# Performance work log

Hardware: AMD Instinct MI355X
Metric: run time of the kernel (lower is better)

## Reference

```python
import jax, jax.numpy as jnp
import numpy as np

DIM = 768
H = 16
HD = DIM // H  # 48


def setup_inputs() -> dict:
    key = jax.random.key(0)
    ks = jax.random.split(key, 9)
    s = 0.02
    return {
        "x": jax.random.normal(ks[0], (8, 1024, DIM), dtype=jnp.float32),
        "w_qkv": jax.random.normal(ks[1], (3 * DIM, DIM), dtype=jnp.float32) * s,
        "b_qkv": jax.random.normal(ks[2], (3 * DIM,), dtype=jnp.float32) * s,
        "w_l": jax.random.normal(ks[3], (H, H), dtype=jnp.float32) * 0.25,
        "b_l": jax.random.normal(ks[4], (H,), dtype=jnp.float32) * s,
        "w_w": jax.random.normal(ks[5], (H, H), dtype=jnp.float32) * 0.25,
        "b_w": jax.random.normal(ks[6], (H,), dtype=jnp.float32) * s,
        "w_proj": jax.random.normal(ks[7], (DIM, DIM), dtype=jnp.float32) * s,
        "b_proj": jax.random.normal(ks[8], (DIM,), dtype=jnp.float32) * s,
    }


def reference(x, w_qkv, b_qkv, w_l, b_l, w_w, b_w, w_proj, b_proj):
    B, N, C = x.shape
    scale = HD ** -0.5
    qkv = x @ w_qkv.T + b_qkv                        # [B,N,3C]
    qkv = qkv.reshape(B, N, 3, H, HD).transpose(2, 0, 3, 1, 4)  # [3,B,H,N,HD]
    q = qkv[0] * scale
    k = qkv[1]
    v = qkv[2]
    attn = jnp.einsum('bhqd,bhkd->bhqk', q, k)       # [B,H,N,N]
    # talking-heads mix before softmax (Linear over head dim)
    attn = jnp.einsum('bhqk,gh->bgqk', attn, w_l) + b_l[None, :, None, None]
    attn = jax.nn.softmax(attn, axis=-1)
    # talking-heads mix after softmax
    attn = jnp.einsum('bhqk,gh->bgqk', attn, w_w) + b_w[None, :, None, None]
    out = jnp.einsum('bhqk,bhkd->bhqd', attn, v)     # [B,H,N,HD]
    out = out.transpose(0, 2, 1, 3).reshape(B, N, C)
    return out @ w_proj.T + b_proj
```

## Files before the change

kernel.cpp:

```cpp
#include <hip/hip_runtime.h>

typedef unsigned short u16;
typedef unsigned int u32;
using short8 = __attribute__((__ext_vector_type__(8))) short;
using f32x4  = __attribute__((__ext_vector_type__(4))) float;

#define DIM 768
#define QKV3 2304
#define SEQ 1024
#define SCALE 0.14433756729740643f

__device__ __forceinline__ u16 f2bf(float f) {
  __bf16 h = (__bf16)f;
  u16 r;
  __builtin_memcpy(&r, &h, 2);
  return r;
}
__device__ __forceinline__ u32 packbf(float lo, float hi) {
  return (u32)f2bf(lo) | ((u32)f2bf(hi) << 16);
}
__device__ __forceinline__ void store1(u16* p, float v) { *p = f2bf(v); }
__device__ __forceinline__ void store1(float* p, float v) { *p = v; }

__device__ __forceinline__ f32x4 mfma16(short8 a, short8 b, f32x4 c) {
  return __builtin_amdgcn_mfma_f32_16x16x32_bf16(a, b, c, 0, 0, 0);
}

__global__ __launch_bounds__(256)
void cvt_f32_bf16(const float* __restrict__ src, u16* __restrict__ dst, int n8) {
  int i = blockIdx.x * 256 + threadIdx.x;
  if (i < n8) {
    float4 a = ((const float4*)src)[2 * i];
    float4 b = ((const float4*)src)[2 * i + 1];
    uint4 o = {packbf(a.x, a.y), packbf(a.z, a.w), packbf(b.x, b.y), packbf(b.z, b.w)};
    ((uint4*)dst)[i] = o;
  }
}

template <typename TO>
__global__ __launch_bounds__(256, 2)
void gemm_bb(const u16* __restrict__ A, const u16* __restrict__ W,
             const float* __restrict__ bias, TO* __restrict__ C,
             int M, int N, int K) {
  __shared__ __align__(16) u16 As[128 * 40];
  __shared__ __align__(16) u16 Bs[128 * 40];
  const int tid = threadIdx.x;
  const int lane = tid & 63;
  const int wv = tid >> 6;
  const int lq = lane & 15;
  const int lc = lane >> 4;
  const int wm = wv >> 1, wn = wv & 1;
  const int row0 = blockIdx.y * 128, col0 = blockIdx.x * 128;

  f32x4 acc[4][4];
#pragma unroll
  for (int i = 0; i < 4; ++i)
#pragma unroll
    for (int j = 0; j < 4; ++j) acc[i][j] = (f32x4){0.f, 0.f, 0.f, 0.f};

  short8 pa[2], pw[2];
  auto issue = [&](int k0) {
#pragma unroll
    for (int t = 0; t < 2; ++t) {
      int id = t * 256 + tid;
      int r = id >> 2, kc = (id & 3) * 8;
      pa[t] = *(const short8*)(A + (size_t)(row0 + r) * K + k0 + kc);
      pw[t] = *(const short8*)(W + (size_t)(col0 + r) * K + k0 + kc);
    }
  };

  issue(0);
#pragma unroll 1
  for (int k0 = 0; k0 < K; k0 += 32) {
    __syncthreads();
#pragma unroll
    for (int t = 0; t < 2; ++t) {
      int id = t * 256 + tid;
      int r = id >> 2, kc = (id & 3) * 8;
      *(short8*)(As + r * 40 + kc) = pa[t];
      *(short8*)(Bs + r * 40 + kc) = pw[t];
    }
    if (k0 + 32 < K) issue(k0 + 32);
    __syncthreads();
    short8 af[4], bf8[4];
#pragma unroll
    for (int i = 0; i < 4; ++i)
      af[i] = *(const short8*)(As + (wm * 64 + i * 16 + lq) * 40 + lc * 8);
#pragma unroll
    for (int j = 0; j < 4; ++j)
      bf8[j] = *(const short8*)(Bs + (wn * 64 + j * 16 + lq) * 40 + lc * 8);
#pragma unroll
    for (int i = 0; i < 4; ++i)
#pragma unroll
      for (int j = 0; j < 4; ++j)
        acc[i][j] = mfma16(af[i], bf8[j], acc[i][j]);
  }
#pragma unroll
  for (int j = 0; j < 4; ++j) {
    int col = col0 + wn * 64 + j * 16 + lq;
    float bv = bias[col];
#pragma unroll
    for (int i = 0; i < 4; ++i)
#pragma unroll
      for (int r = 0; r < 4; ++r) {
        int row = row0 + wm * 64 + i * 16 + lc * 4 + r;
        store1(C + (size_t)row * N + col, acc[i][j][r] + bv);
      }
  }
}

#define KS_ELEMS 24848
#define SMEM_ELEMS 80416
#define ATTN_SMEM 160832

__global__ __launch_bounds__(512, 2)
void attn_kernel(const u16* __restrict__ qkv,
                 const float* __restrict__ wl, const float* __restrict__ bl,
                 const float* __restrict__ ww, const float* __restrict__ bw,
                 u16* __restrict__ obuf) {
  extern __shared__ __align__(16) u16 smem[];
  u16* const Ks0 = smem;
  u16* const Sb  = smem + KS_ELEMS;
  u16* const Vs  = smem + 2 * KS_ELEMS;

  const int tid = threadIdx.x;
  const int wv = tid >> 6;
  const int lane = tid & 63;
  const int lq = lane & 15;
  const int lc = lane >> 4;
  const int b = blockIdx.x >> 5;
  const int qt = blockIdx.x & 31;
  const size_t tokQ = (size_t)b * SEQ + (size_t)qt * 32;
  const size_t tokB = (size_t)b * SEQ;
  const int h0 = wv * 2;

  {
    u32* z = (u32*)smem;
    for (int i = tid; i < SMEM_ELEMS / 2; i += 512) z[i] = 0u;
  }

  short8 qf[2][2][2];
#pragma unroll
  for (int hh = 0; hh < 2; ++hh)
#pragma unroll
    for (int qs = 0; qs < 2; ++qs) {
      const u16* qp = qkv + (tokQ + qs * 16 + lq) * QKV3 + (h0 + hh) * 48;
      qf[hh][qs][0] = *(const short8*)(qp + lc * 8);
      short8 z8 = {0, 0, 0, 0, 0, 0, 0, 0};
      if (lc < 2) z8 = *(const short8*)(qp + 32 + lc * 8);
      qf[hh][qs][1] = z8;
    }

  short8 wlF = {0, 0, 0, 0, 0, 0, 0, 0};
  short8 wwF = {0, 0, 0, 0, 0, 0, 0, 0};
  if (lc < 2) {
#pragma unroll
    for (int e = 0; e < 8; ++e) {
      wlF[e] = (short)f2bf(wl[lq * 16 + lc * 8 + e] * SCALE);
      wwF[e] = (short)f2bf(ww[lq * 16 + lc * 8 + e]);
    }
  }
  float blr[4], bwr[4];
#pragma unroll
  for (int r = 0; r < 4; ++r) { blr[r] = bl[lc * 4 + r]; bwr[r] = bw[lc * 4 + r]; }

  short8 kpre[6], vA[3], vB[3];
  auto issueK = [&](int kt) {
#pragma unroll
    for (int t = 0; t < 6; ++t) {
      int j = t * 512 + tid;
      int kr = j / 96, cc = j - kr * 96;
      kpre[t] = *(const short8*)(qkv + (tokB + (size_t)kt * 32 + kr) * QKV3 + DIM + cc * 8);
    }
  };
  auto issueV = [&](int kt) {
#pragma unroll
    for (int t = 0; t < 3; ++t) {
      int cc = (tid >> 4) + t * 32;
      int kk = tid & 15;
      const u16* v0 = qkv + (tokB + (size_t)kt * 32 + 2 * kk) * QKV3 + 2 * DIM + cc * 8;
      vA[t] = *(const short8*)v0;
      vB[t] = *(const short8*)(v0 + QKV3);
    }
  };
  auto writeK = [&](u16* dst) {
#pragma unroll
    for (int t = 0; t < 6; ++t) {
      int j = t * 512 + tid;
      int kr = j / 96, cc = j - kr * 96;
      *(short8*)(dst + kr * 776 + cc * 8) = kpre[t];
    }
  };
  auto writeV = [&]() {
#pragma unroll
    for (int t = 0; t < 3; ++t) {
      int cc = (tid >> 4) + t * 32;
      int kk = tid & 15;
#pragma unroll
      for (int e = 0; e < 8; ++e)
        *(u32*)(Vs + (cc * 8 + e) * 40 + 2 * kk) =
            (u32)(u16)vA[t][e] | ((u32)(u16)vB[t][e] << 16);
    }
  };
  auto doQK = [&](const u16* kbase) {
#pragma unroll
    for (int ks = 0; ks < 2; ++ks) {
      short8 kf[2][2];
#pragma unroll
      for (int hh = 0; hh < 2; ++hh) {
        const u16* kb = kbase + (ks * 16 + lq) * 776 + (h0 + hh) * 48;
        kf[hh][0] = *(const short8*)(kb + lc * 8);
        kf[hh][1] = *(const short8*)(kb + 32 + lc * 8);
      }
#pragma unroll
      for (int qs = 0; qs < 2; ++qs) {
        f32x4 s0 = {0.f, 0.f, 0.f, 0.f}, s1 = {0.f, 0.f, 0.f, 0.f};
        s0 = mfma16(qf[0][qs][0], kf[0][0], s0);
        s0 = mfma16(qf[0][qs][1], kf[0][1], s0);
        s1 = mfma16(qf[1][qs][0], kf[1][0], s1);
        s1 = mfma16(qf[1][qs][1], kf[1][1], s1);
#pragma unroll
        for (int r = 0; r < 4; ++r) {
          int q = qs * 16 + lc * 4 + r;
          int k = ks * 16 + lq;
          *(u32*)(Sb + q * 776 + k * 24 + h0) = packbf(s0[r], s1[r]);
        }
      }
    }
  };
  auto doPV = [&](f32x4 O[2][3][2]) {
#pragma unroll
    for (int hh = 0; hh < 2; ++hh) {
      const int g2 = h0 + hh;
      short8 w2f[2];
#pragma unroll
      for (int qs = 0; qs < 2; ++qs)
        w2f[qs] = *(const short8*)(Sb + (qs * 16 + lq) * 776 + g2 * 40 + lc * 8);
#pragma unroll
      for (int dt = 0; dt < 3; ++dt) {
        short8 vf = *(const short8*)(Vs + (g2 * 48 + dt * 16 + lq) * 40 + lc * 8);
#pragma unroll
        for (int qs = 0; qs < 2; ++qs)
          O[hh][dt][qs] = mfma16(w2f[qs], vf, O[hh][dt][qs]);
      }
    }
  };

  float Zac[4][4], invZ[4][4];
#pragma unroll
  for (int i = 0; i < 4; ++i)
#pragma unroll
    for (int r = 0; r < 4; ++r) Zac[i][r] = 0.f;

  f32x4 O[2][3][2];
#pragma unroll
  for (int hh = 0; hh < 2; ++hh)
#pragma unroll
    for (int dt = 0; dt < 3; ++dt)
#pragma unroll
      for (int qs = 0; qs < 2; ++qs) O[hh][dt][qs] = (f32x4){0.f, 0.f, 0.f, 0.f};

  issueK(0);
  __syncthreads();
  writeK(Ks0);
  issueK(1);
  __syncthreads();
#pragma unroll 1
  for (int kt = 0; kt < 32; ++kt) {
    u16* cur = (kt & 1) ? Vs : Ks0;
    u16* nxt = (kt & 1) ? Ks0 : Vs;
    if (kt < 31) {
      writeK(nxt);
      issueK(kt == 30 ? 0 : kt + 2);
    }
    doQK(cur);
    __syncthreads();
#pragma unroll
    for (int i = 0; i < 4; ++i) {
      const int q = wv * 4 + i;
      const u16* sq = Sb + q * 776;
#pragma unroll
      for (int ks = 0; ks < 2; ++ks) {
        short8 sf = *(const short8*)(sq + (ks * 16 + lq) * 24 + lc * 8);
        f32x4 cin = {blr[0], blr[1], blr[2], blr[3]};
        f32x4 L = mfma16(wlF, sf, cin);
#pragma unroll
        for (int r = 0; r < 4; ++r) Zac[i][r] += __expf(L[r]);
      }
    }
    __syncthreads();
  }
  issueV(0);
#pragma unroll
  for (int i = 0; i < 4; ++i)
#pragma unroll
    for (int r = 0; r < 4; ++r) {
      float z = Zac[i][r];
      z += __shfl_xor(z, 1);
      z += __shfl_xor(z, 2);
      z += __shfl_xor(z, 4);
      z += __shfl_xor(z, 8);
      invZ[i][r] = 1.0f / z;
    }

#pragma unroll 1
  for (int kt = 0; kt < 32; ++kt) {
    if (kt) doPV(O);
    writeK(Ks0);
    __syncthreads();
    writeV();
    doQK(Ks0);
    if (kt < 31) { issueK(kt + 1); issueV(kt + 1); }
    __syncthreads();
#pragma unroll
    for (int i = 0; i < 4; ++i) {
      const int q = wv * 4 + i;
      u16* const sq = Sb + q * 776;
      f32x4 L[2];
#pragma unroll
      for (int ks = 0; ks < 2; ++ks) {
        short8 sf = *(const short8*)(sq + (ks * 16 + lq) * 24 + lc * 8);
        f32x4 cin = {blr[0], blr[1], blr[2], blr[3]};
        L[ks] = mfma16(wlF, sf, cin);
      }
#pragma unroll
      for (int ks = 0; ks < 2; ++ks) {
        float p0 = __expf(L[ks][0]) * invZ[i][0];
        float p1 = __expf(L[ks][1]) * invZ[i][1];
        float p2 = __expf(L[ks][2]) * invZ[i][2];
        float p3 = __expf(L[ks][3]) * invZ[i][3];
        u16* pp = sq + (ks * 16 + lq) * 24 + lc * 4;
        *(u32*)pp = packbf(p0, p1);
        *(u32*)(pp + 2) = packbf(p2, p3);
      }
      f32x4 W2[2];
#pragma unroll
      for (int ks = 0; ks < 2; ++ks) {
        short8 pf = *(const short8*)(sq + (ks * 16 + lq) * 24 + lc * 8);
        f32x4 cin = {bwr[0], bwr[1], bwr[2], bwr[3]};
        W2[ks] = mfma16(wwF, pf, cin);
      }
#pragma unroll
      for (int ks = 0; ks < 2; ++ks)
#pragma unroll
        for (int r = 0; r < 4; ++r)
          sq[(lc * 4 + r) * 40 + ks * 16 + lq] = f2bf(W2[ks][r]);
    }
    __syncthreads();
  }
  doPV(O);

#pragma unroll
  for (int hh = 0; hh < 2; ++hh)
#pragma unroll
    for (int dt = 0; dt < 3; ++dt)
#pragma unroll
      for (int qs = 0; qs < 2; ++qs)
#pragma unroll
        for (int r = 0; r < 4; ++r) {
          size_t row = tokQ + qs * 16 + lc * 4 + r;
          int col = (h0 + hh) * 48 + dt * 16 + lq;
          obuf[row * DIM + col] = f2bf(O[hh][dt][qs][r]);
        }
}

extern "C" void kernel_launch(void* const* d_in, const int* in_sizes, int n_in,
                              void* d_out, int out_size, void* d_ws, size_t ws_size,
                              hipStream_t stream) {
  const float* x      = (const float*)d_in[0];
  const float* w_qkv  = (const float*)d_in[1];
  const float* b_qkv  = (const float*)d_in[2];
  const float* w_l    = (const float*)d_in[3];
  const float* b_l    = (const float*)d_in[4];
  const float* w_w    = (const float*)d_in[5];
  const float* b_w    = (const float*)d_in[6];
  const float* w_proj = (const float*)d_in[7];
  const float* b_proj = (const float*)d_in[8];
  float* out = (float*)d_out;

  u16* qkv_buf  = (u16*)d_ws;
  u16* attn_buf = qkv_buf + (size_t)8192 * QKV3;
  u16* x_bf     = attn_buf;
  u16* w_qkv_bf  = (u16*)d_out;
  u16* w_proj_bf = qkv_buf;

  static int attr_done = 0;
  if (!attr_done) {
    (void)hipFuncSetAttribute(reinterpret_cast<const void*>(attn_kernel),
                              hipFuncAttributeMaxDynamicSharedMemorySize,
                              ATTN_SMEM);
    attr_done = 1;
  }

  cvt_f32_bf16<<<dim3(864), 256, 0, stream>>>(w_qkv, w_qkv_bf, 221184);
  cvt_f32_bf16<<<dim3(3072), 256, 0, stream>>>(x, x_bf, 786432);
  gemm_bb<u16><<<dim3(QKV3 / 128, 8192 / 128), 256, 0, stream>>>(
      x_bf, w_qkv_bf, b_qkv, qkv_buf, 8192, QKV3, DIM);
  attn_kernel<<<dim3(8 * 32), dim3(512), ATTN_SMEM, stream>>>(
      qkv_buf, w_l, b_l, w_w, b_w, attn_buf);
  cvt_f32_bf16<<<dim3(288), 256, 0, stream>>>(w_proj, w_proj_bf, 73728);
  gemm_bb<float><<<dim3(DIM / 128, 8192 / 128), 256, 0, stream>>>(
      attn_buf, w_proj_bf, b_proj, out, 8192, DIM, DIM);
}
```

Before: 358.1 us.

## Use direct global-to-LDS loads in GEMM and trim attention LDS traffic

The projection GEMM now loads tiles with global_load_lds straight into unpadded shared memory instead of staging through registers, and raises the occupancy hint to four blocks per SM. In the attention kernel, lanes whose MFMA inputs are only zero padding skip their LDS reads. The post-softmax mix swaps MFMA operand order so each lane can write its results as one packed 8-byte store rather than scattered 2-byte stores. Side effects are that the GEMM loses its register prefetch overlap and the unpadded LDS layout may cause bank conflicts.

Measured after the change: 382.4 us. 6.8% more time.

```diff
diff --git a/kernel.cpp b/kernel.cpp
--- a/kernel.cpp
+++ b/kernel.cpp
@@ -24,6 +24,12 @@
 
 __device__ __forceinline__ f32x4 mfma16(short8 a, short8 b, f32x4 c) {
   return __builtin_amdgcn_mfma_f32_16x16x32_bf16(a, b, c, 0, 0, 0);
+}
+
+__device__ __forceinline__ void gload16(const void* g, void* l) {
+  __builtin_amdgcn_global_load_lds(
+      (const __attribute__((address_space(1))) unsigned int*)g,
+      (__attribute__((address_space(3))) unsigned int*)l, 16, 0, 0);
 }
 
 __global__ __launch_bounds__(256)
@@ -38,12 +44,12 @@
 }
 
 template <typename TO>
-__global__ __launch_bounds__(256, 2)
+__global__ __launch_bounds__(256, 4)
 void gemm_bb(const u16* __restrict__ A, const u16* __restrict__ W,
              const float* __restrict__ bias, TO* __restrict__ C,
              int M, int N, int K) {
-  __shared__ __align__(16) u16 As[128 * 40];
-  __shared__ __align__(16) u16 Bs[128 * 40];
+  __shared__ __align__(16) u16 As[128 * 32];
+  __shared__ __align__(16) u16 Bs[128 * 32];
   const int tid = threadIdx.x;
   const int lane = tid & 63;
   const int wv = tid >> 6;
@@ -58,37 +64,24 @@
 #pragma unroll
     for (int j = 0; j < 4; ++j) acc[i][j] = (f32x4){0.f, 0.f, 0.f, 0.f};
 
-  short8 pa[2], pw[2];
-  auto issue = [&](int k0) {
-#pragma unroll
-    for (int t = 0; t < 2; ++t) {
-      int id = t * 256 + tid;
-      int r = id >> 2, kc = (id & 3) * 8;
-      pa[t] = *(const short8*)(A + (size_t)(row0 + r) * K + k0 + kc);
-      pw[t] = *(const short8*)(W + (size_t)(col0 + r) * K + k0 + kc);
-    }
-  };
-
-  issue(0);
 #pragma unroll 1
   for (int k0 = 0; k0 < K; k0 += 32) {
     __syncthreads();
 #pragma unroll
-    for (int t = 0; t < 2; ++t) {
-      int id = t * 256 + tid;
-      int r = id >> 2, kc = (id & 3) * 8;
-      *(short8*)(As + r * 40 + kc) = pa[t];
-      *(short8*)(Bs + r * 40 + kc) = pw[t];
-    }
-    if (k0 + 32 < K) issue(k0 + 32);
+    for (int i = 0; i < 2; ++i) {
+      int c = i * 256 + tid;
+      int r = c >> 2, kc = (c & 3) * 8;
+      gload16(A + (size_t)(row0 + r) * K + k0 + kc, As + c * 8);
+      gload16(W + (size_t)(col0 + r) * K + k0 + kc, Bs + c * 8);
+    }
     __syncthreads();
     short8 af[4], bf8[4];
 #pragma unroll
     for (int i = 0; i < 4; ++i)
-      af[i] = *(const short8*)(As + (wm * 64 + i * 16 + lq) * 40 + lc * 8);
+      af[i] = *(const short8*)(As + (wm * 64 + i * 16 + lq) * 32 + lc * 8);
 #pragma unroll
     for (int j = 0; j < 4; ++j)
-      bf8[j] = *(const short8*)(Bs + (wn * 64 + j * 16 + lq) * 40 + lc * 8);
+      bf8[j] = *(const short8*)(Bs + (wn * 64 + j * 16 + lq) * 32 + lc * 8);
 #pragma unroll
     for (int i = 0; i < 4; ++i)
 #pragma unroll
@@ -133,6 +126,7 @@
   const size_t tokQ = (size_t)b * SEQ + (size_t)qt * 32;
   const size_t tokB = (size_t)b * SEQ;
   const int h0 = wv * 2;
+  const short8 z8 = {0, 0, 0, 0, 0, 0, 0, 0};
 
   {
     u32* z = (u32*)smem;
@@ -146,13 +140,13 @@
     for (int qs = 0; qs < 2; ++qs) {
       const u16* qp = qkv + (tokQ + qs * 16 + lq) * QKV3 + (h0 + hh) * 48;
       qf[hh][qs][0] = *(const short8*)(qp + lc * 8);
-      short8 z8 = {0, 0, 0, 0, 0, 0, 0, 0};
-      if (lc < 2) z8 = *(const short8*)(qp + 32 + lc * 8);
-      qf[hh][qs][1] = z8;
-    }
-
-  short8 wlF = {0, 0, 0, 0, 0, 0, 0, 0};
-  short8 wwF = {0, 0, 0, 0, 0, 0, 0, 0};
+      short8 zq = z8;
+      if (lc < 2) zq = *(const short8*)(qp + 32 + lc * 8);
+      qf[hh][qs][1] = zq;
+    }
+
+  short8 wlF = z8;
+  short8 wwF = z8;
   if (lc < 2) {
 #pragma unroll
     for (int e = 0; e < 8; ++e) {
@@ -160,9 +154,10 @@
       wwF[e] = (short)f2bf(ww[lq * 16 + lc * 8 + e]);
     }
   }
-  float blr[4], bwr[4];
-#pragma unroll
-  for (int r = 0; r < 4; ++r) { blr[r] = bl[lc * 4 + r]; bwr[r] = bw[lc * 4 + r]; }
+  float blr[4];
+#pragma unroll
+  for (int r = 0; r < 4; ++r) blr[r] = bl[lc * 4 + r];
+  const float bwq = bw[lq];
 
   short8 kpre[6], vA[3], vB[3];
   auto issueK = [&](int kt) {
@@ -210,7 +205,9 @@
       for (int hh = 0; hh < 2; ++hh) {
         const u16* kb = kbase + (ks * 16 + lq) * 776 + (h0 + hh) * 48;
         kf[hh][0] = *(const short8*)(kb + lc * 8);
-        kf[hh][1] = *(const short8*)(kb + 32 + lc * 8);
+        short8 k1 = z8;
+        if (lc < 2) k1 = *(const short8*)(kb + 32 + lc * 8);
+        kf[hh][1] = k1;
       }
 #pragma unroll
       for (int qs = 0; qs < 2; ++qs) {
@@ -281,7 +278,8 @@
       const u16* sq = Sb + q * 776;
 #pragma unroll
       for (int ks = 0; ks < 2; ++ks) {
-        short8 sf = *(const short8*)(sq + (ks * 16 + lq) * 24 + lc * 8);
+        short8 sf = z8;
+        if (lc < 2) sf = *(const short8*)(sq + (ks * 16 + lq) * 24 + lc * 8);
         f32x4 cin = {blr[0], blr[1], blr[2], blr[3]};
         f32x4 L = mfma16(wlF, sf, cin);
 #pragma unroll
@@ -319,7 +317,8 @@
       f32x4 L[2];
 #pragma unroll
       for (int ks = 0; ks < 2; ++ks) {
-        short8 sf = *(const short8*)(sq + (ks * 16 + lq) * 24 + lc * 8);
+        short8 sf = z8;
+        if (lc < 2) sf = *(const short8*)(sq + (ks * 16 + lq) * 24 + lc * 8);
         f32x4 cin = {blr[0], blr[1], blr[2], blr[3]};
         L[ks] = mfma16(wlF, sf, cin);
       }
@@ -329,22 +328,22 @@
         float p1 = __expf(L[ks][1]) * invZ[i][1];
         float p2 = __expf(L[ks][2]) * invZ[i][2];
         float p3 = __expf(L[ks][3]) * invZ[i][3];
-        u16* pp = sq + (ks * 16 + lq) * 24 + lc * 4;
-        *(u32*)pp = packbf(p0, p1);
-        *(u32*)(pp + 2) = packbf(p2, p3);
+        uint2 pv = {packbf(p0, p1), packbf(p2, p3)};
+        *(uint2*)(sq + (ks * 16 + lq) * 24 + lc * 4) = pv;
       }
       f32x4 W2[2];
+      f32x4 cw = {bwq, bwq, bwq, bwq};
 #pragma unroll
       for (int ks = 0; ks < 2; ++ks) {
-        short8 pf = *(const short8*)(sq + (ks * 16 + lq) * 24 + lc * 8);
-        f32x4 cin = {bwr[0], bwr[1], bwr[2], bwr[3]};
-        W2[ks] = mfma16(wwF, pf, cin);
-      }
-#pragma unroll
-      for (int ks = 0; ks < 2; ++ks)
-#pragma unroll
-        for (int r = 0; r < 4; ++r)
-          sq[(lc * 4 + r) * 40 + ks * 16 + lq] = f2bf(W2[ks][r]);
+        short8 pf = z8;
+        if (lc < 2) pf = *(const short8*)(sq + (ks * 16 + lq) * 24 + lc * 8);
+        W2[ks] = mfma16(pf, wwF, cw);
+      }
+#pragma unroll
+      for (int ks = 0; ks < 2; ++ks) {
+        uint2 wv2 = {packbf(W2[ks][0], W2[ks][1]), packbf(W2[ks][2], W2[ks][3])};
+        *(uint2*)(sq + lq * 40 + ks * 16 + lc * 4) = wv2;
+      }
     }
     __syncthreads();
   }
```
